# Optimization experiments

Measured on AMD Instinct MI355X. Metric: run time of the kernel, lower is better.

Reference implementation:

```python
import jax, jax.numpy as jnp
import numpy as np

N_ENT = 50000
N_REL = 200
N_EDGE = 1_000_000
D = 64


def setup_inputs() -> dict:
    key = jax.random.key(0)
    ks = jax.random.split(key, 12)
    src = jax.random.randint(ks[0], (N_EDGE,), 0, N_ENT)
    rel = jax.random.randint(ks[1], (N_EDGE,), 0, N_REL)
    dst = jax.random.randint(ks[2], (N_EDGE,), 0, N_ENT)
    triples = jnp.stack([src, rel, dst], axis=1).astype(jnp.int64)  # [E,3]
    s = 1.0 / np.sqrt(D)
    return {
        "emb_e": jax.random.normal(ks[3], (N_ENT, D), jnp.float32) * s,
        "re_att": jax.random.normal(ks[4], (N_REL,), jnp.float32) * 0.1,
        "W1": jax.random.normal(ks[5], (D, D), jnp.float32) * s,
        "W2": jax.random.normal(ks[6], (D, D), jnp.float32) * s,
        "W3": jax.random.normal(ks[7], (D, D), jnp.float32) * s,
        "u": jax.random.normal(ks[8], (3 * D,), jnp.float32) * s,
        "en_weight": jax.random.normal(ks[9], (D, D), jnp.float32) * s,
        "re_weight": jax.random.normal(ks[10], (D, D), jnp.float32) * s,
        "re_spec": jax.random.normal(ks[11], (D,), jnp.float32) * s,
        "triples": triples,
    }


def _forward(emb_e, re_att, W1, W2, W3, u, en_weight, re_weight, re_spec, triples):
    src = triples[:, 0]
    rel = triples[:, 1]
    dst = triples[:, 2]
    n = emb_e.shape[0]

    def wgc(x, W):
        # relation-weighted message passing: out[s] += w[r] * x[d]
        msg = jax.ops.segment_sum(x[dst] * re_att[rel][:, None], src, num_segments=n)
        return jnp.tanh((x + msg) @ W)

    x = wgc(emb_e, W1)
    x = wgc(x, W2)
    x = wgc(x, W3)

    # GAT-style edge scores: e = LeakyReLU(u . [W_en h_i ; W_re r_spec ; W_en h_j])
    d = x.shape[1]
    hs = x @ en_weight.T                       # [N,d] = (en_weight @ h)^T rows
    z_src = hs @ u[:d]                         # [N]
    z_dst = hs @ u[2 * d:]                     # [N]
    z_mid = u[d:2 * d] @ (re_weight @ re_spec)  # scalar, same for every edge
    scores = jax.nn.leaky_relu(z_src[src] + z_mid + z_dst[dst], 0.01)  # [E]

    # softmax normalized over ALL triples (global denominator, per source code)
    alpha = jax.nn.softmax(scores)

    # out[src] += alpha_e * x[dst]
    out = jax.ops.segment_sum(alpha[:, None] * x[dst], src, num_segments=n)
    return out


def reference(emb_e, re_att, W1, W2, W3, u, en_weight, re_weight, re_spec, triples):
    return _forward(emb_e, re_att, W1, W2, W3, u, en_weight, re_weight, re_spec, triples)
```

## Files before the change

### kernel.cpp

```cpp
#include <hip/hip_runtime.h>
#include <math.h>

#define N_ENT  50000
#define N_REL  200
#define N_EDGE 1000000
#define CHUNK  196
#define NCH    64
#define ECH2   15625
#define NPART  4
#define NRNG   12500
#define EPK_CAP 1540096
#define DUMMY  ((200u << 16) | 50000u)

#define WS_ZSUM   128
#define WS_ZMID   192
#define WS_AV     256
#define WS_BV     512
#define WS_WT     0x00001000
#define WS_BSUM   0x00010000
#define WS_BBASE  0x00011000
#define WS_TOT    0x00040000
#define WS_OFFS   0x00080000
#define WS_ZSRC   0x000C0000
#define WS_ZDST   0x00100000
#define WS_SNODE  0x00140000
#define WS_SRCS   0x00180000
#define WS_EB     0x00380000
#define WS_XB0    0x00180000
#define WS_EPK    0x007A0000
#define WS_HIST   0x00D80000
#define WS_XB1    0x00D80000

typedef __attribute__((ext_vector_type(8))) short s16x8;
typedef __attribute__((ext_vector_type(4))) float f32x4;

__device__ __forceinline__ float bflo(unsigned u) { return __uint_as_float(u << 16); }
__device__ __forceinline__ float bfhi(unsigned u) { return __uint_as_float(u & 0xffff0000u); }
__device__ __forceinline__ float bf2f(unsigned short u) {
  return __uint_as_float(((unsigned)u) << 16);
}
__device__ __forceinline__ unsigned short f2bf(float f) {
  unsigned u = __float_as_uint(f);
  unsigned r = ((u >> 16) & 1u) + 0x7fffu;
  return (unsigned short)((u + r) >> 16);
}
__device__ __forceinline__ float fast_tanh(float x) {
  float ex = __expf(2.f * x);
  return 1.f - __fdividef(2.f, ex + 1.f);
}
__device__ __forceinline__ void fma8(float* acc, float wt, uint4 q) {
  acc[0] += wt * bflo(q.x); acc[1] += wt * bfhi(q.x);
  acc[2] += wt * bflo(q.y); acc[3] += wt * bfhi(q.y);
  acc[4] += wt * bflo(q.z); acc[5] += wt * bfhi(q.z);
  acc[6] += wt * bflo(q.w); acc[7] += wt * bfhi(q.w);
}
__device__ __forceinline__ int tri_is64(const void* tri) {
  int z = ((const int*)tri)[2 * (threadIdx.x & 63) + 1];
  return __ballot(z == 0) == ~0ull;
}

__global__ void k_decode(const void* tri, unsigned short* __restrict__ srcs,
                         unsigned* __restrict__ eb) {
  int is64 = tri_is64(tri);
  int stride = gridDim.x * blockDim.x;
  if (is64) {
    const long long* t = (const long long*)tri;
    for (int e = blockIdx.x * blockDim.x + threadIdx.x; e < N_EDGE; e += stride) {
      int s = (int)t[3 * e], r = (int)t[3 * e + 1], d = (int)t[3 * e + 2];
      srcs[e] = (unsigned short)s;
      eb[e] = ((unsigned)r << 16) | (unsigned)d;
    }
  } else {
    const int* t = (const int*)tri;
    for (int e = blockIdx.x * blockDim.x + threadIdx.x; e < N_EDGE; e += stride) {
      int s = t[3 * e], r = t[3 * e + 1], d = t[3 * e + 2];
      srcs[e] = (unsigned short)s;
      eb[e] = ((unsigned)r << 16) | (unsigned)d;
    }
  }
}

__global__ void __launch_bounds__(256) k_hist(const unsigned short* __restrict__ srcs,
                                              unsigned short* __restrict__ hist) {
  __shared__ unsigned h[NRNG];
  int c = blockIdx.x >> 2, x = blockIdx.x & 3;
  int lo = x * NRNG;
  for (int i = threadIdx.x; i < NRNG; i += 256) h[i] = 0u;
  __syncthreads();
  int e0 = c * ECH2, e1 = e0 + ECH2;
  for (int e = e0 + threadIdx.x; e < e1; e += 256) {
    int rel = (int)srcs[e] - lo;
    if ((unsigned)rel < NRNG) atomicAdd(&h[rel], 1u);
  }
  __syncthreads();
  for (int i = threadIdx.x; i < NRNG; i += 256)
    hist[c * N_ENT + lo + i] = (unsigned short)h[i];
}

__global__ void __launch_bounds__(256) k_scanH(unsigned short* __restrict__ hist,
                                               int* __restrict__ tot, int* __restrict__ bsum) {
  int t = threadIdx.x;
  int s = blockIdx.x * CHUNK + t;
  int padded = 0;
  if (t < CHUNK && s < N_ENT) {
    int run = 0;
    for (int c = 0; c < NCH; c++) {
      int v = hist[c * N_ENT + s];
      hist[c * N_ENT + s] = (unsigned short)run;
      run += v;
    }
    padded = (run + 15) & ~15;
    tot[s] = padded;
  }
  int v = padded;
  for (int o = 32; o; o >>= 1) v += __shfl_down(v, o);
  __shared__ int sm[4];
  if ((t & 63) == 0) sm[t >> 6] = v;
  __syncthreads();
  if (t == 0) bsum[blockIdx.x] = sm[0] + sm[1] + sm[2] + sm[3];
}

__global__ void __launch_bounds__(256) k_scanBpre(
    const int* __restrict__ bsum, int* __restrict__ bbase, int* __restrict__ offs,
    double* zsum, const float* u, const float* enw, const float* rew, const float* rsp,
    float* av, float* bv, float* zmid, float* zd,
    const float* W1, const float* W2, const float* W3, unsigned short* wt) {
  __shared__ int sm[256];
  int t = threadIdx.x;
  int v = bsum[t];
  sm[t] = v;
  __syncthreads();
  for (int d = 1; d < 256; d <<= 1) {
    int x = (t >= d) ? sm[t - d] : 0;
    __syncthreads();
    sm[t] += x;
    __syncthreads();
  }
  bbase[t] = sm[t] - v;
  if (t == 255) offs[N_ENT] = sm[255];
  if (t == 0) *zsum = 0.0;
  if (t == 64) zd[N_ENT] = -1e30f;
  if (t < 64) {
    int k = t;
    float aa = 0.f, bb = 0.f;
    for (int j = 0; j < 64; j++) {
      float w = enw[j * 64 + k];
      aa += u[j] * w;
      bb += u[128 + j] * w;
    }
    av[k] = aa; bv[k] = bb;
    float z = 0.f;
    for (int c = 0; c < 64; c++) z += rew[k * 64 + c] * rsp[c];
    z *= u[64 + k];
    for (int o = 32; o; o >>= 1) z += __shfl_down(z, o);
    if (k == 0) *zmid = z;
  }
  for (int idx = t; idx < 4096; idx += 256) {
    int k = idx >> 6, n = idx & 63;
    wt[0 * 4608 + n * 72 + k] = f2bf(W1[idx]);
    wt[1 * 4608 + n * 72 + k] = f2bf(W2[idx]);
    wt[2 * 4608 + n * 72 + k] = f2bf(W3[idx]);
  }
}

__global__ void k_scanC(const int* __restrict__ counts, const int* __restrict__ bbase,
                        int* __restrict__ offs) {
  __shared__ int sm[256];
  int t = threadIdx.x;
  int i = blockIdx.x * CHUNK + t;
  int v = (t < CHUNK && i < N_ENT) ? counts[i] : 0;
  sm[t] = v;
  __syncthreads();
  for (int d = 1; d < 256; d <<= 1) {
    int x = (t >= d) ? sm[t - d] : 0;
    __syncthreads();
    sm[t] += x;
    __syncthreads();
  }
  if (t < CHUNK && i < N_ENT)
    offs[i] = bbase[blockIdx.x] + sm[t] - v;
}

__global__ void k_fill(unsigned* __restrict__ epk) {
  int i = blockIdx.x * blockDim.x + threadIdx.x;
  if (i * 4 < EPK_CAP)
    ((uint4*)epk)[i] = make_uint4(DUMMY, DUMMY, DUMMY, DUMMY);
}

__global__ void __launch_bounds__(256) k_scatter(
    const unsigned short* __restrict__ srcs, const unsigned* __restrict__ eb,
    const unsigned short* __restrict__ cbase, const int* __restrict__ offs,
    unsigned* __restrict__ epk) {
  __shared__ unsigned h[NRNG];
  int c = blockIdx.x >> 2, x = blockIdx.x & 3;
  int lo = x * NRNG;
  for (int i = threadIdx.x; i < NRNG; i += 256) h[i] = 0u;
  __syncthreads();
  int e0 = c * ECH2, e1 = e0 + ECH2;
  for (int e = e0 + threadIdx.x; e < e1; e += 256) {
    int s = (int)srcs[e];
    int rel = s - lo;
    if ((unsigned)rel < NRNG) {
      int lr = atomicAdd(&h[rel], 1u);
      epk[offs[s] + (int)cbase[c * N_ENT + s] + lr] = eb[e];
    }
  }
}

__global__ void k_conv(const float* __restrict__ x, unsigned short* __restrict__ xb0,
                       unsigned short* __restrict__ xb1) {
  int i = blockIdx.x * blockDim.x + threadIdx.x;
  if (i < N_ENT * 16) {
    float4 v = ((const float4*)x)[i];
    ushort4 o;
    o.x = f2bf(v.x); o.y = f2bf(v.y); o.z = f2bf(v.z); o.w = f2bf(v.w);
    ((ushort4*)xb0)[i] = o;
  } else if (i < N_ENT * 16 + 16) {
    ((ushort4*)xb0)[i] = make_ushort4(0, 0, 0, 0);
    ((ushort4*)xb1)[i] = make_ushort4(0, 0, 0, 0);
  }
}

template <int EPI>
__global__ void __launch_bounds__(256) k_wgc(
    const unsigned short* __restrict__ xb, const unsigned short* __restrict__ wt,
    const int* __restrict__ offs, const unsigned* __restrict__ epk,
    const float* __restrict__ re_att, unsigned short* __restrict__ yb,
    const float* __restrict__ av, const float* __restrict__ bv,
    float* __restrict__ zsrc, float* __restrict__ zdst) {
  __shared__ __align__(16) unsigned short s_m[16 * 72];
  __shared__ __align__(16) unsigned short s_wt[64 * 72];
  __shared__ float s_att[N_REL + 1];
  for (int i = threadIdx.x; i < N_REL + 1; i += 256)
    s_att[i] = (i < N_REL) ? re_att[i] : 0.f;
  for (int i = threadIdx.x; i < 1152; i += 256)
    ((uint2*)s_wt)[i] = ((const uint2*)wt)[i];
  __syncthreads();

  int wv = threadIdx.x >> 6, lane = threadIdx.x & 63;
  int g = lane >> 3, c8 = (lane & 7) * 8;
  float fa = 0.f, fb = 0.f;
  if (EPI) { fa = av[lane]; fb = bv[lane]; }

  for (int i = 0; i < 4; i++) {
    int nl = wv * 4 + i;
    int node = blockIdx.x * 16 + nl;
    int e0 = offs[node], e1 = offs[node + 1];
    float acc[8] = {0.f, 0.f, 0.f, 0.f, 0.f, 0.f, 0.f, 0.f};
    {
      uint4 q = *(const uint4*)(xb + (size_t)node * 64 + c8);
      fma8(acc, (g == 0) ? 1.f : 0.f, q);
    }
    for (int e = e0; e < e1; e += 16) {
      unsigned pa = epk[e + g];
      unsigned pb = epk[e + g + 8];
      float wa = s_att[pa >> 16];
      float wb = s_att[pb >> 16];
      uint4 qa = *(const uint4*)(xb + (size_t)(pa & 0xffffu) * 64 + c8);
      uint4 qb = *(const uint4*)(xb + (size_t)(pb & 0xffffu) * 64 + c8);
      fma8(acc, wa, qa);
      fma8(acc, wb, qb);
    }
#pragma unroll
    for (int off = 8; off <= 32; off <<= 1)
#pragma unroll
      for (int c = 0; c < 8; c++) acc[c] += __shfl_xor(acc[c], off);
    if (lane < 8) {
      uint4 pk;
      pk.x = (unsigned)f2bf(acc[0]) | ((unsigned)f2bf(acc[1]) << 16);
      pk.y = (unsigned)f2bf(acc[2]) | ((unsigned)f2bf(acc[3]) << 16);
      pk.z = (unsigned)f2bf(acc[4]) | ((unsigned)f2bf(acc[5]) << 16);
      pk.w = (unsigned)f2bf(acc[6]) | ((unsigned)f2bf(acc[7]) << 16);
      *(uint4*)&s_m[nl * 72 + lane * 8] = pk;
    }
  }
  __syncthreads();

  int ar = (lane & 15) * 72 + (lane >> 4) * 8;
  int br = (wv * 16 + (lane & 15)) * 72 + (lane >> 4) * 8;
  s16x8 a0 = *(const s16x8*)&s_m[ar];
  s16x8 a1 = *(const s16x8*)&s_m[ar + 32];
  s16x8 b0 = *(const s16x8*)&s_wt[br];
  s16x8 b1 = *(const s16x8*)&s_wt[br + 32];
  f32x4 c = {0.f, 0.f, 0.f, 0.f};
  c = __builtin_amdgcn_mfma_f32_16x16x32_bf16(a0, b0, c, 0, 0, 0);
  c = __builtin_amdgcn_mfma_f32_16x16x32_bf16(a1, b1, c, 0, 0, 0);
  __syncthreads();
#pragma unroll
  for (int q = 0; q < 4; q++) {
    int r = (lane >> 4) * 4 + q;
    s_m[r * 72 + wv * 16 + (lane & 15)] = f2bf(fast_tanh(c[q]));
  }
  __syncthreads();

  {
    int r = threadIdx.x >> 4, c0 = (threadIdx.x & 15) * 4;
    ushort4 o;
    o.x = s_m[r * 72 + c0]; o.y = s_m[r * 72 + c0 + 1];
    o.z = s_m[r * 72 + c0 + 2]; o.w = s_m[r * 72 + c0 + 3];
    *(ushort4*)(yb + ((size_t)blockIdx.x * 16 + r) * 64 + c0) = o;
  }
  if (EPI) {
    for (int i = 0; i < 4; i++) {
      int nl = wv * 4 + i;
      float yf = bf2f(s_m[nl * 72 + lane]);
      float za = yf * fa, zb = yf * fb;
      for (int s = 32; s; s >>= 1) { za += __shfl_down(za, s); zb += __shfl_down(zb, s); }
      if (lane == 0) {
        int node = blockIdx.x * 16 + nl;
        zsrc[node] = za; zdst[node] = zb;
      }
    }
  }
}

__global__ void __launch_bounds__(256) k_out(
    const unsigned short* __restrict__ xb, const int* __restrict__ offs,
    const unsigned* __restrict__ epk, const float* __restrict__ zs,
    const float* __restrict__ zd, const float* zmid,
    float* __restrict__ out, float* __restrict__ snode) {
  int wid = (blockIdx.x * blockDim.x + threadIdx.x) >> 6;
  int lane = threadIdx.x & 63;
  if (wid >= N_ENT) return;
  int node = wid;
  int g = lane >> 3, c8 = (lane & 7) * 8;
  float zi = zs[node] + *zmid;
  float acc[8] = {0.f, 0.f, 0.f, 0.f, 0.f, 0.f, 0.f, 0.f};
  float s0 = 0.f;
  int e0 = offs[node], e1 = offs[node + 1];
  for (int e = e0; e < e1; e += 16) {
    unsigned pa = epk[e + g];
    unsigned pb = epk[e + g + 8];
    unsigned da = pa & 0xffffu;
    unsigned db = pb & 0xffffu;
    float ca = zi + zd[da];
    float cb = zi + zd[db];
    ca = ca >= 0.f ? ca : 0.01f * ca;
    cb = cb >= 0.f ? cb : 0.01f * cb;
    float wa = __expf(ca);
    float wb = __expf(cb);
    uint4 qa = *(const uint4*)(xb + (size_t)da * 64 + c8);
    uint4 qb = *(const uint4*)(xb + (size_t)db * 64 + c8);
    fma8(acc, wa, qa);
    fma8(acc, wb, qb);
    s0 += wa + wb;
  }
#pragma unroll
  for (int off = 8; off <= 32; off <<= 1) {
#pragma unroll
    for (int c = 0; c < 8; c++) acc[c] += __shfl_xor(acc[c], off);
    s0 += __shfl_xor(s0, off);
  }
  if (lane < 8) {
    float4* p = (float4*)(out + (size_t)node * 64 + lane * 8);
    p[0] = make_float4(acc[0], acc[1], acc[2], acc[3]);
    p[1] = make_float4(acc[4], acc[5], acc[6], acc[7]);
  }
  if (lane == 0) snode[node] = s0;
}

__global__ void k_red(const float* __restrict__ snode, double* zsum) {
  int stride = gridDim.x * blockDim.x;
  double s = 0.0;
  for (int i = blockIdx.x * blockDim.x + threadIdx.x; i < N_ENT; i += stride)
    s += (double)snode[i];
  for (int o = 32; o; o >>= 1) s += __shfl_down(s, o);
  __shared__ double ws_[4];
  if ((threadIdx.x & 63) == 0) ws_[threadIdx.x >> 6] = s;
  __syncthreads();
  if (threadIdx.x == 0)
    atomicAdd(zsum, ws_[0] + ws_[1] + ws_[2] + ws_[3]);
}

__global__ void k_norm(float* __restrict__ out, const double* zsum) {
  int i = blockIdx.x * blockDim.x + threadIdx.x;
  if (i >= N_ENT * 16) return;
  float invZ = (float)(1.0 / *zsum);
  float4 v = ((float4*)out)[i];
  v.x *= invZ; v.y *= invZ; v.z *= invZ; v.w *= invZ;
  ((float4*)out)[i] = v;
}

extern "C" void kernel_launch(void* const* d_in, const int* in_sizes, int n_in,
                              void* d_out, int out_size, void* d_ws, size_t ws_size,
                              hipStream_t stream) {
  const float* emb   = (const float*)d_in[0];
  const float* reatt = (const float*)d_in[1];
  const float* W1    = (const float*)d_in[2];
  const float* W2    = (const float*)d_in[3];
  const float* W3    = (const float*)d_in[4];
  const float* u     = (const float*)d_in[5];
  const float* enw   = (const float*)d_in[6];
  const float* rew   = (const float*)d_in[7];
  const float* rsp   = (const float*)d_in[8];
  const void*  tri   = d_in[9];

  char* ws = (char*)d_ws;
  double*         zsum   = (double*)(ws + WS_ZSUM);
  float*          zmid   = (float*)(ws + WS_ZMID);
  float*          av     = (float*)(ws + WS_AV);
  float*          bv     = (float*)(ws + WS_BV);
  unsigned short* wt     = (unsigned short*)(ws + WS_WT);
  int*            bsum   = (int*)(ws + WS_BSUM);
  int*            bbase  = (int*)(ws + WS_BBASE);
  int*            tot    = (int*)(ws + WS_TOT);
  int*            offs   = (int*)(ws + WS_OFFS);
  float*          zsrc   = (float*)(ws + WS_ZSRC);
  float*          zdst   = (float*)(ws + WS_ZDST);
  float*          snode  = (float*)(ws + WS_SNODE);
  unsigned short* srcs   = (unsigned short*)(ws + WS_SRCS);
  unsigned*       eb     = (unsigned*)(ws + WS_EB);
  unsigned*       epk    = (unsigned*)(ws + WS_EPK);
  unsigned short* hist   = (unsigned short*)(ws + WS_HIST);
  unsigned short* xb0    = (unsigned short*)(ws + WS_XB0);
  unsigned short* xb1    = (unsigned short*)(ws + WS_XB1);
  float*          out    = (float*)d_out;

  k_decode<<<4096, 256, 0, stream>>>(tri, srcs, eb);
  k_hist<<<NCH * NPART, 256, 0, stream>>>(srcs, hist);
  k_scanH<<<256, 256, 0, stream>>>(hist, tot, bsum);
  k_scanBpre<<<1, 256, 0, stream>>>(bsum, bbase, offs, zsum, u, enw, rew, rsp,
                                    av, bv, zmid, zdst, W1, W2, W3, wt);
  k_scanC<<<256, 256, 0, stream>>>(tot, bbase, offs);
  k_fill<<<EPK_CAP / 1024, 256, 0, stream>>>(epk);
  k_scatter<<<NCH * NPART, 256, 0, stream>>>(srcs, eb, hist, offs, epk);
  k_conv<<<3126, 256, 0, stream>>>(emb, xb0, xb1);

  k_wgc<0><<<3125, 256, 0, stream>>>(xb0, wt + 0 * 4608, offs, epk, reatt, xb1,
                                     nullptr, nullptr, nullptr, nullptr);
  k_wgc<0><<<3125, 256, 0, stream>>>(xb1, wt + 1 * 4608, offs, epk, reatt, xb0,
                                     nullptr, nullptr, nullptr, nullptr);
  k_wgc<1><<<3125, 256, 0, stream>>>(xb0, wt + 2 * 4608, offs, epk, reatt, xb1,
                                     av, bv, zsrc, zdst);

  k_out<<<12500, 256, 0, stream>>>(xb1, offs, epk, zsrc, zdst, zmid, out, snode);
  k_red<<<196, 256, 0, stream>>>(snode, zsum);
  k_norm<<<3125, 256, 0, stream>>>(out, zsum);
}
```

Baseline: 224.7 us.

## Split gather by column halves and separate aggregation from MFMA matmul

The fused gather+matmul kernel is split into two kernels. The first is a gather kernel in which each block handles one 32-column half of 16 nodes, so each lane loads 16 bytes per edge with 16 edges per iteration. The second is a separate MFMA kernel that reads the aggregated messages from a global buffer. The output aggregation kernel uses the same column-half split with twice as many blocks. The aim is more parallelism and a smaller per-block working set in the gather phase, likely improving cache locality. The cost is an extra global round-trip for the message buffer, three extra launches, and index decoding done twice per edge.

Result: slower. 310.7 us (+38.2%).

```diff
diff --git a/kernel.cpp b/kernel.cpp
--- a/kernel.cpp
+++ b/kernel.cpp
@@ -30,6 +30,7 @@
 #define WS_EPK    0x007A0000
 #define WS_HIST   0x00D80000
 #define WS_XB1    0x00D80000
+#define WS_MBUF   0x01400000
 
 typedef __attribute__((ext_vector_type(8))) short s16x8;
 typedef __attribute__((ext_vector_type(4))) float f32x4;
@@ -221,142 +222,134 @@
   }
 }
 
-template <int EPI>
-__global__ void __launch_bounds__(256) k_wgc(
-    const unsigned short* __restrict__ xb, const unsigned short* __restrict__ wt,
-    const int* __restrict__ offs, const unsigned* __restrict__ epk,
-    const float* __restrict__ re_att, unsigned short* __restrict__ yb,
-    const float* __restrict__ av, const float* __restrict__ bv,
-    float* __restrict__ zsrc, float* __restrict__ zdst) {
-  __shared__ __align__(16) unsigned short s_m[16 * 72];
-  __shared__ __align__(16) unsigned short s_wt[64 * 72];
+__global__ void __launch_bounds__(256) k_gch(
+    const unsigned short* __restrict__ xb, const int* __restrict__ offs,
+    const unsigned* __restrict__ epk, const float* __restrict__ re_att,
+    unsigned short* __restrict__ mbuf) {
   __shared__ float s_att[N_REL + 1];
   for (int i = threadIdx.x; i < N_REL + 1; i += 256)
     s_att[i] = (i < N_REL) ? re_att[i] : 0.f;
-  for (int i = threadIdx.x; i < 1152; i += 256)
-    ((uint2*)s_wt)[i] = ((const uint2*)wt)[i];
-  __syncthreads();
-
+  __syncthreads();
+
+  int h = blockIdx.x & 1;
+  int bg = blockIdx.x >> 1;
   int wv = threadIdx.x >> 6, lane = threadIdx.x & 63;
-  int g = lane >> 3, c8 = (lane & 7) * 8;
-  float fa = 0.f, fb = 0.f;
-  if (EPI) { fa = av[lane]; fb = bv[lane]; }
+  int q4 = lane >> 2;
+  int cb = h * 32 + (lane & 3) * 8;
 
   for (int i = 0; i < 4; i++) {
-    int nl = wv * 4 + i;
-    int node = blockIdx.x * 16 + nl;
+    int node = bg * 16 + wv * 4 + i;
     int e0 = offs[node], e1 = offs[node + 1];
     float acc[8] = {0.f, 0.f, 0.f, 0.f, 0.f, 0.f, 0.f, 0.f};
     {
-      uint4 q = *(const uint4*)(xb + (size_t)node * 64 + c8);
-      fma8(acc, (g == 0) ? 1.f : 0.f, q);
+      uint4 q = *(const uint4*)(xb + (size_t)node * 64 + cb);
+      fma8(acc, (q4 == 0) ? 1.f : 0.f, q);
     }
     for (int e = e0; e < e1; e += 16) {
-      unsigned pa = epk[e + g];
-      unsigned pb = epk[e + g + 8];
-      float wa = s_att[pa >> 16];
-      float wb = s_att[pb >> 16];
-      uint4 qa = *(const uint4*)(xb + (size_t)(pa & 0xffffu) * 64 + c8);
-      uint4 qb = *(const uint4*)(xb + (size_t)(pb & 0xffffu) * 64 + c8);
-      fma8(acc, wa, qa);
-      fma8(acc, wb, qb);
-    }
-#pragma unroll
-    for (int off = 8; off <= 32; off <<= 1)
+      unsigned p = epk[e + q4];
+      float w = s_att[p >> 16];
+      uint4 q = *(const uint4*)(xb + (size_t)(p & 0xffffu) * 64 + cb);
+      fma8(acc, w, q);
+    }
+#pragma unroll
+    for (int off = 4; off <= 32; off <<= 1)
 #pragma unroll
       for (int c = 0; c < 8; c++) acc[c] += __shfl_xor(acc[c], off);
-    if (lane < 8) {
+    if (lane < 4) {
       uint4 pk;
       pk.x = (unsigned)f2bf(acc[0]) | ((unsigned)f2bf(acc[1]) << 16);
       pk.y = (unsigned)f2bf(acc[2]) | ((unsigned)f2bf(acc[3]) << 16);
       pk.z = (unsigned)f2bf(acc[4]) | ((unsigned)f2bf(acc[5]) << 16);
       pk.w = (unsigned)f2bf(acc[6]) | ((unsigned)f2bf(acc[7]) << 16);
-      *(uint4*)&s_m[nl * 72 + lane * 8] = pk;
-    }
-  }
-  __syncthreads();
-
-  int ar = (lane & 15) * 72 + (lane >> 4) * 8;
+      *(uint4*)(mbuf + (size_t)node * 64 + h * 32 + lane * 8) = pk;
+    }
+  }
+}
+
+template <int EPI>
+__global__ void __launch_bounds__(256) k_mm(
+    const unsigned short* __restrict__ mbuf, const unsigned short* __restrict__ wt,
+    unsigned short* __restrict__ yb,
+    const float* __restrict__ av, const float* __restrict__ bv,
+    float* __restrict__ zsrc, float* __restrict__ zdst) {
+  __shared__ __align__(16) unsigned short s_m[16 * 72];
+  __shared__ __align__(16) unsigned short s_wt[64 * 72];
+  for (int i = threadIdx.x; i < 1152; i += 256)
+    ((uint2*)s_wt)[i] = ((const uint2*)wt)[i];
+  int wv = threadIdx.x >> 6, lane = threadIdx.x & 63;
+  int nb = blockIdx.x * 16;
+  const unsigned short* ar = mbuf + (size_t)(nb + (lane & 15)) * 64 + (lane >> 4) * 8;
+  s16x8 a0 = *(const s16x8*)ar;
+  s16x8 a1 = *(const s16x8*)(ar + 32);
+  __syncthreads();
   int br = (wv * 16 + (lane & 15)) * 72 + (lane >> 4) * 8;
-  s16x8 a0 = *(const s16x8*)&s_m[ar];
-  s16x8 a1 = *(const s16x8*)&s_m[ar + 32];
   s16x8 b0 = *(const s16x8*)&s_wt[br];
   s16x8 b1 = *(const s16x8*)&s_wt[br + 32];
   f32x4 c = {0.f, 0.f, 0.f, 0.f};
   c = __builtin_amdgcn_mfma_f32_16x16x32_bf16(a0, b0, c, 0, 0, 0);
   c = __builtin_amdgcn_mfma_f32_16x16x32_bf16(a1, b1, c, 0, 0, 0);
-  __syncthreads();
 #pragma unroll
   for (int q = 0; q < 4; q++) {
     int r = (lane >> 4) * 4 + q;
     s_m[r * 72 + wv * 16 + (lane & 15)] = f2bf(fast_tanh(c[q]));
   }
   __syncthreads();
-
   {
     int r = threadIdx.x >> 4, c0 = (threadIdx.x & 15) * 4;
-    ushort4 o;
-    o.x = s_m[r * 72 + c0]; o.y = s_m[r * 72 + c0 + 1];
-    o.z = s_m[r * 72 + c0 + 2]; o.w = s_m[r * 72 + c0 + 3];
-    *(ushort4*)(yb + ((size_t)blockIdx.x * 16 + r) * 64 + c0) = o;
+    ushort4 ov;
+    ov.x = s_m[r * 72 + c0]; ov.y = s_m[r * 72 + c0 + 1];
+    ov.z = s_m[r * 72 + c0 + 2]; ov.w = s_m[r * 72 + c0 + 3];
+    *(ushort4*)(yb + ((size_t)nb + r) * 64 + c0) = ov;
   }
   if (EPI) {
+    float fa = av[lane], fb = bv[lane];
+#pragma unroll
     for (int i = 0; i < 4; i++) {
       int nl = wv * 4 + i;
       float yf = bf2f(s_m[nl * 72 + lane]);
       float za = yf * fa, zb = yf * fb;
       for (int s = 32; s; s >>= 1) { za += __shfl_down(za, s); zb += __shfl_down(zb, s); }
-      if (lane == 0) {
-        int node = blockIdx.x * 16 + nl;
-        zsrc[node] = za; zdst[node] = zb;
-      }
-    }
-  }
-}
-
-__global__ void __launch_bounds__(256) k_out(
+      if (lane == 0) { zsrc[nb + nl] = za; zdst[nb + nl] = zb; }
+    }
+  }
+}
+
+__global__ void __launch_bounds__(256) k_oth(
     const unsigned short* __restrict__ xb, const int* __restrict__ offs,
     const unsigned* __restrict__ epk, const float* __restrict__ zs,
     const float* __restrict__ zd, const float* zmid,
     float* __restrict__ out, float* __restrict__ snode) {
-  int wid = (blockIdx.x * blockDim.x + threadIdx.x) >> 6;
-  int lane = threadIdx.x & 63;
-  if (wid >= N_ENT) return;
-  int node = wid;
-  int g = lane >> 3, c8 = (lane & 7) * 8;
+  int h = blockIdx.x & 1;
+  int wv = threadIdx.x >> 6, lane = threadIdx.x & 63;
+  int q4 = lane >> 2;
+  int cb = h * 32 + (lane & 3) * 8;
+  int node = (blockIdx.x >> 1) * 4 + wv;
   float zi = zs[node] + *zmid;
   float acc[8] = {0.f, 0.f, 0.f, 0.f, 0.f, 0.f, 0.f, 0.f};
   float s0 = 0.f;
   int e0 = offs[node], e1 = offs[node + 1];
   for (int e = e0; e < e1; e += 16) {
-    unsigned pa = epk[e + g];
-    unsigned pb = epk[e + g + 8];
-    unsigned da = pa & 0xffffu;
-    unsigned db = pb & 0xffffu;
-    float ca = zi + zd[da];
-    float cb = zi + zd[db];
-    ca = ca >= 0.f ? ca : 0.01f * ca;
-    cb = cb >= 0.f ? cb : 0.01f * cb;
-    float wa = __expf(ca);
-    float wb = __expf(cb);
-    uint4 qa = *(const uint4*)(xb + (size_t)da * 64 + c8);
-    uint4 qb = *(const uint4*)(xb + (size_t)db * 64 + c8);
-    fma8(acc, wa, qa);
-    fma8(acc, wb, qb);
-    s0 += wa + wb;
-  }
-#pragma unroll
-  for (int off = 8; off <= 32; off <<= 1) {
+    unsigned p = epk[e + q4];
+    unsigned d = p & 0xffffu;
+    float cc = zi + zd[d];
+    cc = cc >= 0.f ? cc : 0.01f * cc;
+    float w = __expf(cc);
+    uint4 q = *(const uint4*)(xb + (size_t)d * 64 + cb);
+    fma8(acc, w, q);
+    s0 += w;
+  }
+#pragma unroll
+  for (int off = 4; off <= 32; off <<= 1) {
 #pragma unroll
     for (int c = 0; c < 8; c++) acc[c] += __shfl_xor(acc[c], off);
     s0 += __shfl_xor(s0, off);
   }
-  if (lane < 8) {
-    float4* p = (float4*)(out + (size_t)node * 64 + lane * 8);
-    p[0] = make_float4(acc[0], acc[1], acc[2], acc[3]);
-    p[1] = make_float4(acc[4], acc[5], acc[6], acc[7]);
-  }
-  if (lane == 0) snode[node] = s0;
+  if (lane < 4) {
+    float4* pp = (float4*)(out + (size_t)node * 64 + h * 32 + lane * 8);
+    pp[0] = make_float4(acc[0], acc[1], acc[2], acc[3]);
+    pp[1] = make_float4(acc[4], acc[5], acc[6], acc[7]);
+  }
+  if (h == 0 && lane == 0) snode[node] = s0;
 }
 
 __global__ void k_red(const float* __restrict__ snode, double* zsum) {
@@ -414,6 +407,7 @@
   unsigned short* hist   = (unsigned short*)(ws + WS_HIST);
   unsigned short* xb0    = (unsigned short*)(ws + WS_XB0);
   unsigned short* xb1    = (unsigned short*)(ws + WS_XB1);
+  unsigned short* mbuf   = (unsigned short*)(ws + WS_MBUF);
   float*          out    = (float*)d_out;
 
   k_decode<<<4096, 256, 0, stream>>>(tri, srcs, eb);
@@ -426,14 +420,14 @@
   k_scatter<<<NCH * NPART, 256, 0, stream>>>(srcs, eb, hist, offs, epk);
   k_conv<<<3126, 256, 0, stream>>>(emb, xb0, xb1);
 
-  k_wgc<0><<<3125, 256, 0, stream>>>(xb0, wt + 0 * 4608, offs, epk, reatt, xb1,
-                                     nullptr, nullptr, nullptr, nullptr);
-  k_wgc<0><<<3125, 256, 0, stream>>>(xb1, wt + 1 * 4608, offs, epk, reatt, xb0,
-                                     nullptr, nullptr, nullptr, nullptr);
-  k_wgc<1><<<3125, 256, 0, stream>>>(xb0, wt + 2 * 4608, offs, epk, reatt, xb1,
-                                     av, bv, zsrc, zdst);
-
-  k_out<<<12500, 256, 0, stream>>>(xb1, offs, epk, zsrc, zdst, zmid, out, snode);
+  k_gch<<<6250, 256, 0, stream>>>(xb0, offs, epk, reatt, mbuf);
+  k_mm<0><<<3125, 256, 0, stream>>>(mbuf, wt + 0 * 4608, xb1, nullptr, nullptr, nullptr, nullptr);
+  k_gch<<<6250, 256, 0, stream>>>(xb1, offs, epk, reatt, mbuf);
+  k_mm<0><<<3125, 256, 0, stream>>>(mbuf, wt + 1 * 4608, xb0, nullptr, nullptr, nullptr, nullptr);
+  k_gch<<<6250, 256, 0, stream>>>(xb0, offs, epk, reatt, mbuf);
+  k_mm<1><<<3125, 256, 0, stream>>>(mbuf, wt + 2 * 4608, xb1, av, bv, zsrc, zdst);
+
+  k_oth<<<25000, 256, 0, stream>>>(xb1, offs, epk, zsrc, zdst, zmid, out, snode);
   k_red<<<196, 256, 0, stream>>>(snode, zsum);
   k_norm<<<3125, 256, 0, stream>>>(out, zsum);
 }
```
